# Optimization experiments

Hardware: AMD Instinct MI355X
Metric: run time of the kernel (lower is better)

The kernel has to match this reference:

```python
import jax, jax.numpy as jnp
import numpy as np

B, S, D, H, E = 4, 1024, 1024, 16, 4
HD = D // H
EPS = 1e-5


def setup_inputs() -> dict:
    key = jax.random.key(0)
    ks = jax.random.split(key, 6)
    std = 0.02
    return {
        "hidden_states": jax.random.normal(ks[0], (B, S, D), dtype=jnp.float32),
        "Wr": jax.random.normal(ks[1], (D, E), dtype=jnp.float32) * std,
        "br": jnp.zeros((E,), jnp.float32),
        "ln_g": jnp.ones((E, D), jnp.float32),
        "ln_b": jnp.zeros((E, D), jnp.float32),
        "W_attn": jax.random.normal(ks[2], (E, D, 3 * D), dtype=jnp.float32) * std,
        "b_attn": jnp.zeros((E, 3 * D), jnp.float32),
        "W_proj": jax.random.normal(ks[3], (E, D, D), dtype=jnp.float32) * std,
        "b_proj": jnp.zeros((E, D), jnp.float32),
    }


def reference(hidden_states, Wr, br, ln_g, ln_b, W_attn, b_attn, W_proj, b_proj):
    b, s, d = hidden_states.shape
    x = hidden_states.reshape(b * s, d)  # [N, D]

    # naive softmax router over experts
    score = jax.nn.softmax(x @ Wr + br, axis=-1)  # [N, E]

    # LayerNorm stats are expert-independent; affine is per-expert
    mu = jnp.mean(x, axis=-1, keepdims=True)
    var = jnp.mean(jnp.square(x - mu), axis=-1, keepdims=True)
    xn = (x - mu) * jax.lax.rsqrt(var + EPS)  # [N, D]

    ln_out = xn[:, None, :] * ln_g[None] + ln_b[None]  # [N, E, D]
    qkv_all = jnp.einsum('ned,edf->nef', ln_out, W_attn) + b_attn  # [N, E, 3D]
    # weighted_qkv: scale each expert's qkv by its routing score, sum
    qkv = jnp.einsum('ne,nef->nf', score, qkv_all)  # [N, 3D]

    q, k, v = jnp.split(qkv.reshape(b, s, 3 * d), 3, axis=-1)
    def split_heads(t):
        return t.reshape(b, s, H, HD).transpose(0, 2, 1, 3)  # [B,H,S,hd]
    q, k, v = split_heads(q), split_heads(k), split_heads(v)

    scale = 1.0 / jnp.sqrt(jnp.asarray(HD, q.dtype))
    att = jnp.einsum('bhqd,bhkd->bhqk', q, k) * scale  # [B,H,S,S]
    causal = jnp.tril(jnp.ones((s, s), dtype=bool))
    att = jnp.where(causal[None, None], att, jnp.finfo(att.dtype).min)
    probs = jax.nn.softmax(att, axis=-1)
    ctx = jnp.einsum('bhqk,bhkd->bhqd', probs, v)  # [B,H,S,hd]
    ctx = ctx.transpose(0, 2, 1, 3).reshape(b * s, d)  # [N, D]

    proj_all = jnp.einsum('nd,edf->nef', ctx, W_proj) + b_proj  # [N, E, D]
    out = jnp.einsum('ne,nef->nf', score, proj_all).reshape(b, s, d)
    return out
```

## Files before the change

kernel.cpp:

```cpp
#include <hip/hip_runtime.h>
#include <stdint.h>

#define NB 4
#define SS 1024
#define DD 1024
#define EE 4
#define HH 16
#define HDD 64
#define NN (NB*SS)
#define KK2 (EE*DD)
#define FF1 (3*DD)

typedef __attribute__((ext_vector_type(4))) float f32x4;
typedef __attribute__((ext_vector_type(8))) _Float16 half8;
typedef __attribute__((ext_vector_type(4))) _Float16 half4;

static __device__ __forceinline__ f32x4 mfma16(half8 a, half8 b, f32x4 c){
  return __builtin_amdgcn_mfma_f32_16x16x32_f16(a, b, c, 0, 0, 0);
}

#define GLOAD_LDS16(gp, lp) __builtin_amdgcn_global_load_lds( \
    (const unsigned int __attribute__((address_space(1)))*)(uintptr_t)(gp), \
    (unsigned int __attribute__((address_space(3)))*)(uintptr_t)(lp), 16, 0, 0)

#define SBAR() do { asm volatile("" ::: "memory"); \
                    __builtin_amdgcn_s_barrier(); \
                    asm volatile("" ::: "memory"); } while(0)
#define VMC(n) asm volatile("s_waitcnt vmcnt(" #n ")" ::: "memory")

__device__ __forceinline__ void prep_body(
    const float* __restrict__ x, const float* __restrict__ Wr,
    const float* __restrict__ br, float* __restrict__ score,
    float* __restrict__ ratios, _Float16* __restrict__ xnb,
    int n, float (*red)[6])
{
  int tid = threadIdx.x;
  float4 xv = ((const float4*)(x + (size_t)n*DD))[tid];
  float xa[4] = {xv.x, xv.y, xv.z, xv.w};
  float vals[6];
  vals[0] = xa[0]+xa[1]+xa[2]+xa[3];
  vals[1] = xa[0]*xa[0]+xa[1]*xa[1]+xa[2]*xa[2]+xa[3]*xa[3];
  vals[2] = vals[3] = vals[4] = vals[5] = 0.f;
  #pragma unroll
  for (int j = 0; j < 4; ++j){
    float4 w = ((const float4*)Wr)[tid*4 + j];
    vals[2] += xa[j]*w.x; vals[3] += xa[j]*w.y;
    vals[4] += xa[j]*w.z; vals[5] += xa[j]*w.w;
  }
  #pragma unroll
  for (int off = 32; off >= 1; off >>= 1)
    #pragma unroll
    for (int i = 0; i < 6; ++i)
      vals[i] += __shfl_xor(vals[i], off, 64);
  int wid = tid >> 6;
  if ((tid & 63) == 0){
    #pragma unroll
    for (int i = 0; i < 6; ++i) red[wid][i] = vals[i];
  }
  __syncthreads();
  float tot[6];
  #pragma unroll
  for (int i = 0; i < 6; ++i)
    tot[i] = red[0][i] + red[1][i] + red[2][i] + red[3][i];

  float mu   = tot[0] * (1.f/DD);
  float var  = tot[1] * (1.f/DD) - mu*mu;
  float rsig = rsqrtf(var + 1e-5f);
  float lg[4];
  #pragma unroll
  for (int e = 0; e < 4; ++e) lg[e] = tot[2+e] + br[e];
  float mx = fmaxf(fmaxf(lg[0], lg[1]), fmaxf(lg[2], lg[3]));
  float ex[4], esum = 0.f;
  #pragma unroll
  for (int e = 0; e < 4; ++e){ ex[e] = __expf(lg[e] - mx); esum += ex[e]; }
  if (tid < 4){
    score[n*4 + tid] = ex[tid] / esum;
    ratios[n*4 + tid] = (tid == 0) ? (ex[0] / esum) : (ex[tid] / ex[tid-1]);
  }

  half4 o;
  #pragma unroll
  for (int j = 0; j < 4; ++j) o[j] = (_Float16)((xa[j] - mu) * rsig);
  *(half4*)(xnb + (size_t)n*DD + tid*4) = o;
}

template<bool AFFINE>
__device__ __forceinline__ void transpose_body(
    const float* __restrict__ W, _Float16* __restrict__ WT, int K, int F,
    const float* __restrict__ gvec, const float* __restrict__ bvec,
    float* __restrict__ part, int k0, int f0,
    float (*t)[65], float (*red2)[64])
{
  int tid = threadIdx.x;
  int r = tid >> 4, c4 = (tid & 15) * 4;
  float pf[4] = {0.f, 0.f, 0.f, 0.f};
  #pragma unroll
  for (int i = 0; i < 4; ++i){
    int k = k0 + i*16 + r;
    float4 v = *(const float4*)(W + (size_t)k*F + f0 + c4);
    if constexpr (AFFINE){
      float bk = bvec[k];
      pf[0] += bk*v.x; pf[1] += bk*v.y; pf[2] += bk*v.z; pf[3] += bk*v.w;
      float gk = gvec[k];
      v.x *= gk; v.y *= gk; v.z *= gk; v.w *= gk;
    }
    t[i*16 + r][c4+0] = v.x; t[i*16 + r][c4+1] = v.y;
    t[i*16 + r][c4+2] = v.z; t[i*16 + r][c4+3] = v.w;
  }
  if constexpr (AFFINE){
    #pragma unroll
    for (int j = 0; j < 4; ++j) red2[r][c4+j] = pf[j];
  }
  __syncthreads();
  int f = tid >> 2, seg = tid & 3;
  half8 o0, o1;
  #pragma unroll
  for (int j = 0; j < 8; ++j){
    o0[j] = (_Float16)t[seg*16 + j][f];
    o1[j] = (_Float16)t[seg*16 + 8 + j][f];
  }
  _Float16* dst = WT + (size_t)(f0 + f)*K + k0 + seg*16;
  *(half8*)dst = o0;
  *(half8*)(dst + 8) = o1;
  if constexpr (AFFINE){
    if (tid < 64){
      float s = 0.f;
      #pragma unroll
      for (int rr = 0; rr < 16; ++rr) s += red2[rr][tid];
      part[(size_t)(k0/64) * F + f0 + tid] = s;
    }
  }
}

__global__ __launch_bounds__(256) void prep_fused_kernel(
    const float* __restrict__ W1, _Float16* __restrict__ W1T,
    const float* __restrict__ W2, _Float16* __restrict__ W2T,
    const float* __restrict__ gvec, const float* __restrict__ bvec,
    float* __restrict__ part,
    const float* __restrict__ x, const float* __restrict__ Wr,
    const float* __restrict__ br, float* __restrict__ score,
    float* __restrict__ ratios, _Float16* __restrict__ xnb)
{
  __shared__ float t[64][65];
  __shared__ float red2[16][64];
  __shared__ float red[4][6];
  int id = blockIdx.x;
  if (id & 1){
    prep_body(x, Wr, br, score, ratios, xnb, id >> 1, red);
  } else {
    int tr = id >> 1;
    int k0 = (tr & 63) * 64;
    int y  = tr >> 6;
    if (y < FF1/64)
      transpose_body<true >(W1, W1T, KK2, FF1, gvec, bvec, part, k0, y*64, t, red2);
    else
      transpose_body<false>(W2, W2T, KK2, DD, nullptr, nullptr, nullptr,
                            k0, (y - FF1/64)*64, t, red2);
  }
}

__global__ __launch_bounds__(256) void bb1_kernel(
    const float* __restrict__ b_attn, const float* __restrict__ part,
    float* __restrict__ BB1)
{
  int idx = blockIdx.x*256 + threadIdx.x;
  int e = idx / FF1, f = idx - e*FF1;
  float s = b_attn[idx];
  #pragma unroll
  for (int i = 0; i < 16; ++i)
    s += part[(size_t)(e*16 + i)*FF1 + f];
  BB1[idx] = s;
}

#define G1_BM 256
#define G1_BN 192
#define G1_BK 64
#define G1_NT 16
#define G1_ABUF (G1_BM*G1_BK)
#define G1_BBUF (G1_BN*G1_BK)

__global__ __launch_bounds__(512, 2) void gemm1_kernel(
    const _Float16* __restrict__ XN, const _Float16* __restrict__ BT,
    const float* __restrict__ score, const float* __restrict__ ratios,
    const float* __restrict__ bias, _Float16* __restrict__ C)
{
  __shared__ _Float16 smA[2*G1_ABUF];
  __shared__ _Float16 smB[3*G1_BBUF];
  int tid = threadIdx.x;
  int lane = tid & 63, wid = tid >> 6;
  int q = lane & 15, g = lane >> 4;
  int wr = wid >> 1, wc = wid & 1;
  int xo = (q & 7) << 3;
  int bid = blockIdx.x;
  int xcd = bid & 7, li = bid >> 3;
  int m0 = (li >> 1) * G1_BM;
  int n0 = (xcd*2 + (li & 1)) * G1_BN;

  int arow[4], brow[6];
  #pragma unroll
  for (int mf = 0; mf < 4; ++mf) arow[mf] = (wr*64 + mf*16 + q)*64;
  #pragma unroll
  for (int nf = 0; nf < 6; ++nf) brow[nf] = (wc*96 + nf*16 + q)*64;
  int soff[2] = { (g*8) ^ xo, (32 + g*8) ^ xo };

  _Float16 rf[4][4];
  #pragma unroll
  for (int mf = 0; mf < 4; ++mf){
    float4 rr = *(const float4*)(ratios + (size_t)(m0 + wr*64 + mf*16 + q)*4);
    rf[mf][0] = (_Float16)rr.x; rf[mf][1] = (_Float16)rr.y;
    rf[mf][2] = (_Float16)rr.z; rf[mf][3] = (_Float16)rr.w;
  }

  auto stageA = [&](int t){
    _Float16* sA = smA + (t & 1)*G1_ABUF;
    const int d0 = t * G1_BK;
    #pragma unroll
    for (int ld = 0; ld < 4; ++ld){
      int c = ld*512 + tid;
      int row = c >> 3;
      int seg = (c & 7) ^ (row & 7);
      GLOAD_LDS16(XN + (size_t)(m0 + row)*DD + d0 + seg*8,
                  sA + (ld*512 + wid*64)*8);
    }
  };
  auto stageB = [&](int gec){
    const int k0 = (gec & 3)*DD + (gec >> 2)*G1_BK;
    _Float16* sB = smB + (gec % 3)*G1_BBUF;
    #pragma unroll
    for (int ld = 0; ld < 3; ++ld){
      int c = ld*512 + tid;
      int row = c >> 3;
      int seg = (c & 7) ^ (row & 7);
      GLOAD_LDS16(BT + (size_t)(n0 + row)*KK2 + k0 + seg*8,
                  sB + (ld*512 + wid*64)*8);
    }
  };

  f32x4 acc[4][6] = {};
  half8 af[4][2];

  auto phase = [&](const _Float16* Ab, const _Float16* Bb,
                   _Float16 s0, _Float16 s1, _Float16 s2, _Float16 s3,
                   bool readAF){
    if (readAF){
      #pragma unroll
      for (int m = 0; m < 4; ++m)
        #pragma unroll
        for (int k = 0; k < 2; ++k)
          af[m][k] = *(const half8*)(Ab + arow[m] + soff[k]);
    }
    #pragma unroll
    for (int k = 0; k < 2; ++k)
      #pragma unroll
      for (int j = 0; j < 8; ++j){
        af[0][k][j] *= s0; af[1][k][j] *= s1;
        af[2][k][j] *= s2; af[3][k][j] *= s3;
      }
    half8 bf[3][2];
    #pragma unroll
    for (int n = 0; n < 3; ++n)
      #pragma unroll
      for (int k = 0; k < 2; ++k)
        bf[n][k] = *(const half8*)(Bb + brow[n] + soff[k]);
    __builtin_amdgcn_s_setprio(1);
    #pragma unroll
    for (int k = 0; k < 2; ++k)
      #pragma unroll
      for (int m = 0; m < 4; ++m)
        #pragma unroll
        for (int n = 0; n < 3; ++n)
          acc[m][n] = mfma16(af[m][k], bf[n][k], acc[m][n]);
    __builtin_amdgcn_s_setprio(0);
    #pragma unroll
    for (int n = 0; n < 3; ++n)
      #pragma unroll
      for (int k = 0; k < 2; ++k)
        bf[n][k] = *(const half8*)(Bb + brow[3+n] + soff[k]);
    __builtin_amdgcn_s_setprio(1);
    #pragma unroll
    for (int k = 0; k < 2; ++k)
      #pragma unroll
      for (int m = 0; m < 4; ++m)
        #pragma unroll
        for (int n = 0; n < 3; ++n)
          acc[m][3+n] = mfma16(af[m][k], bf[n][k], acc[m][3+n]);
    __builtin_amdgcn_s_setprio(0);
  };

  stageA(0); stageB(0); stageB(1);

  #pragma unroll 1
  for (int t = 0; t < G1_NT-1; ++t){
    const _Float16* Ab = smA + (t & 1)*G1_ABUF;
    int g4 = t*4;
    VMC(3); SBAR();
    stageB(g4+2);
    phase(Ab, smB + (g4 % 3)*G1_BBUF, rf[0][0], rf[1][0], rf[2][0], rf[3][0], true);
    VMC(3); SBAR();
    stageB(g4+3);
    phase(Ab, smB + ((g4+1) % 3)*G1_BBUF, rf[0][1], rf[1][1], rf[2][1], rf[3][1], false);
    VMC(3); SBAR();
    stageB(g4+4); stageA(t+1);
    phase(Ab, smB + ((g4+2) % 3)*G1_BBUF, rf[0][2], rf[1][2], rf[2][2], rf[3][2], false);
    VMC(7); SBAR();
    stageB(g4+5);
    phase(Ab, smB + ((g4+3) % 3)*G1_BBUF, rf[0][3], rf[1][3], rf[2][3], rf[3][3], false);
  }
  {
    const _Float16* Ab = smA + ((G1_NT-1) & 1)*G1_ABUF;
    VMC(3); SBAR();
    stageB(62);
    phase(Ab, smB + (60 % 3)*G1_BBUF, rf[0][0], rf[1][0], rf[2][0], rf[3][0], true);
    VMC(3); SBAR();
    stageB(63);
    phase(Ab, smB + (61 % 3)*G1_BBUF, rf[0][1], rf[1][1], rf[2][1], rf[3][1], false);
    VMC(3); SBAR();
    phase(Ab, smB + (62 % 3)*G1_BBUF, rf[0][2], rf[1][2], rf[2][2], rf[3][2], false);
    VMC(0); SBAR();
    phase(Ab, smB + (63 % 3)*G1_BBUF, rf[0][3], rf[1][3], rf[2][3], rf[3][3], false);
  }

  float bv[6][4];
  #pragma unroll
  for (int nf = 0; nf < 6; ++nf){
    int gn = n0 + wc*96 + nf*16 + q;
    #pragma unroll
    for (int e = 0; e < 4; ++e) bv[nf][e] = bias[e*FF1 + gn];
  }
  #pragma unroll
  for (int mf = 0; mf < 4; ++mf){
    #pragma unroll
    for (int r = 0; r < 4; ++r){
      int gm = m0 + wr*64 + mf*16 + g*4 + r;
      float4 sc = *(const float4*)(score + gm*4);
      #pragma unroll
      for (int nf = 0; nf < 6; ++nf){
        int gn = n0 + wc*96 + nf*16 + q;
        float v = acc[mf][nf][r]
                + sc.x*bv[nf][0] + sc.y*bv[nf][1] + sc.z*bv[nf][2] + sc.w*bv[nf][3];
        C[(size_t)gm*FF1 + gn] = (_Float16)v;
      }
    }
  }
}

#define G2_BK 64
#define G2_ABUF (128*G2_BK)
#define G2_BUFSZ (2*G2_ABUF)

__global__ __launch_bounds__(512) void gemm2_kernel(
    const _Float16* __restrict__ CTX, const _Float16* __restrict__ BT,
    const float* __restrict__ score, const float* __restrict__ bias,
    float* __restrict__ Cout)
{
  __shared__ _Float16 smem[2*G2_BUFSZ];
  int tid = threadIdx.x;
  int lane = tid & 63, wid = tid >> 6;
  int q = lane & 15, g = lane >> 4;
  int wr = wid >> 2, wc = wid & 3;
  int xo = (q & 7) << 3;
  int bid = blockIdx.x;
  int xcd = bid >> 5, idx = bid & 31;
  int m0 = (xcd*4 + (idx >> 3)) * 128;
  int n0 = (idx & 7) * 128;

  int arow[4], brow[2];
  #pragma unroll
  for (int mf = 0; mf < 4; ++mf) arow[mf] = (wr*64 + mf*16 + q)*64;
  #pragma unroll
  for (int nf = 0; nf < 2; ++nf) brow[nf] = G2_ABUF + (wc*32 + nf*16 + q)*64;
  int soff[2] = { (g*8) ^ xo, (32 + g*8) ^ xo };

  auto stage = [&](int t, int buf){
    const int d0 = (t & 15) * G2_BK;
    const int k0 = t * G2_BK;
    _Float16* sA = smem + buf*G2_BUFSZ;
    _Float16* sB = sA + G2_ABUF;
    #pragma unroll
    for (int ld = 0; ld < 2; ++ld){
      int c = ld*512 + tid;
      int row = c >> 3;
      int seg = (c & 7) ^ (row & 7);
      GLOAD_LDS16(CTX + (size_t)(m0 + row)*DD + d0 + seg*8,
                  sA + (ld*512 + wid*64)*8);
    }
    #pragma unroll
    for (int ld = 0; ld < 2; ++ld){
      int c = ld*512 + tid;
      int row = c >> 3;
      int seg = (c & 7) ^ (row & 7);
      GLOAD_LDS16(BT + (size_t)(n0 + row)*KK2 + k0 + seg*8,
                  sB + (ld*512 + wid*64)*8);
    }
  };

  f32x4 accp[4][2] = {}, acco[4][2] = {};

  auto merge = [&](int e){
    #pragma unroll
    for (int m = 0; m < 4; ++m)
      #pragma unroll
      for (int r = 0; r < 4; ++r){
        int gm = m0 + wr*64 + m*16 + g*4 + r;
        float s = score[(size_t)gm*4 + e];
        #pragma unroll
        for (int n = 0; n < 2; ++n){
          acco[m][n][r] += s*accp[m][n][r];
          accp[m][n][r] = 0.f;
        }
      }
  };

  half8 af[4][2], bfr[2][2];
  auto reads = [&](const _Float16* base, int k){
    #pragma unroll
    for (int m = 0; m < 4; ++m)
      af[m][k] = *(const half8*)(base + arow[m] + soff[k]);
    #pragma unroll
    for (int n = 0; n < 2; ++n)
      bfr[n][k] = *(const half8*)(base + brow[n] + soff[k]);
  };
  auto mfmas = [&](int k){
    __builtin_amdgcn_s_setprio(1);
    #pragma unroll
    for (int m = 0; m < 4; ++m)
      #pragma unroll
      for (int n = 0; n < 2; ++n)
        accp[m][n] = mfma16(af[m][k], bfr[n][k], accp[m][n]);
    __builtin_amdgcn_s_setprio(0);
  };

  stage(0, 0);
  for (int t = 0; t < KK2/G2_BK - 1; ++t){
    const _Float16* base = smem + (t & 1)*G2_BUFSZ;
    stage(t+1, (t+1)&1);
    asm volatile("s_waitcnt vmcnt(4)" ::: "memory");
    SBAR();
    reads(base, 0);
    mfmas(0);
    reads(base, 1);
    SBAR();
    mfmas(1);
    if ((t & 15) == 15) merge(t >> 4);
  }
  {
    const _Float16* base = smem + ((KK2/G2_BK - 1) & 1)*G2_BUFSZ;
    asm volatile("s_waitcnt vmcnt(0)" ::: "memory");
    SBAR();
    reads(base, 0); reads(base, 1);
    mfmas(0); mfmas(1);
    merge(3);
  }

  #pragma unroll
  for (int m = 0; m < 4; ++m){
    #pragma unroll
    for (int r = 0; r < 4; ++r){
      int gm = m0 + wr*64 + m*16 + g*4 + r;
      float4 sc = *(const float4*)(score + gm*4);
      #pragma unroll
      for (int n = 0; n < 2; ++n){
        int gn = n0 + wc*32 + n*16 + q;
        float v = acco[m][n][r]
                + sc.x*bias[gn] + sc.y*bias[DD+gn]
                + sc.z*bias[2*DD+gn] + sc.w*bias[3*DD+gn];
        Cout[(size_t)gm*DD + gn] = v;
      }
    }
  }
}

__global__ __launch_bounds__(512) void attn_kernel(
    const _Float16* __restrict__ qkv, _Float16* __restrict__ ctx)
{
  __shared__ _Float16 lsK[2][64*64];
  __shared__ _Float16 lsV[2][64*64];
  __shared__ _Float16 lsP[8][16*64];
  int id = blockIdx.x;
  int p = id >> 1, parity = id & 1;
  int bh = p & 63;
  int qtp = p >> 6;
  int qt = parity ? qtp : 7 - qtp;
  int b = bh >> 4, h = bh & 15;
  int tid = threadIdx.x, lane = tid & 63, wid = tid >> 6;
  int q = lane & 15, g = lane >> 4;
  int xo = (q & 7) << 3;
  int qrow0 = qt*128 + wid*16;

  half8 qf[2];
  #pragma unroll
  for (int kk = 0; kk < 2; ++kk)
    qf[kk] = *(const half8*)(qkv + ((size_t)b*SS + qrow0 + q)*FF1 + h*HDD + kk*32 + g*8);

  auto issueK = [&](int kt, int buf){
    size_t kvrow = (size_t)b*SS + kt*64;
    int row = tid >> 3, seg = (tid & 7) ^ (row & 7);
    GLOAD_LDS16(qkv + (kvrow + row)*FF1 + DD + h*HDD + seg*8,
                lsK[buf] + (size_t)(wid*64)*8);
  };
  auto issueV = [&](int kt, half8& vr){
    size_t kvrow = (size_t)b*SS + kt*64;
    vr = *(const half8*)(qkv + (kvrow + lane)*FF1 + 2*DD + h*HDD + wid*8);
  };
  auto writeV = [&](half8 vr, int buf){
    #pragma unroll
    for (int j = 0; j < 8; ++j){
      int hd = wid*8 + j;
      lsV[buf][hd*64 + (lane ^ ((hd & 7) << 3))] = vr[j];
    }
  };

  f32x4 o[4] = {};
  float mrow = -1e30f, lsum = 0.f;
  const float SC2 = 0.18033688011112042f;
  int qglob = qrow0 + q;
  int ktmax = 2*qt + 1;

  half8 vr;
  issueK(0, 0);
  issueV(0, vr);

  for (int kt = 0; kt <= ktmax; ++kt){
    int cur = kt & 1, nxt = cur ^ 1;
    int tn = (kt < ktmax) ? kt+1 : ktmax;
    bool active = (kt*64 <= qrow0 + 15);
    asm volatile("s_waitcnt vmcnt(1)" ::: "memory");
    SBAR();

    f32x4 st[4] = {};
    if (active){
      __builtin_amdgcn_s_setprio(1);
      #pragma unroll
      for (int i = 0; i < 4; ++i){
        #pragma unroll
        for (int kk = 0; kk < 2; ++kk){
          half8 kf = *(const half8*)(lsK[cur] + (i*16 + q)*64 + ((kk*32 + g*8) ^ xo));
          st[i] = mfma16(kf, qf[kk], st[i]);
        }
      }
      __builtin_amdgcn_s_setprio(0);
    }
    issueK(tn, nxt);
    asm volatile("s_waitcnt vmcnt(1)" ::: "memory");
    writeV(vr, cur);

    _Float16 pb[16];
    bool resc = false;
    float psum = 0.f;
    if (active){
      float pvv[16]; float tm = -1e30f;
      if (kt*64 + 63 > qrow0){
        #pragma unroll
        for (int i = 0; i < 4; ++i)
          #pragma unroll
          for (int r = 0; r < 4; ++r){
            int kglob = kt*64 + i*16 + g*4 + r;
            float sv = (kglob <= qglob) ? st[i][r]*SC2 : -1e30f;
            pvv[i*4+r] = sv; tm = fmaxf(tm, sv);
          }
      } else {
        #pragma unroll
        for (int i = 0; i < 4; ++i)
          #pragma unroll
          for (int r = 0; r < 4; ++r){
            float sv = st[i][r]*SC2;
            pvv[i*4+r] = sv; tm = fmaxf(tm, sv);
          }
      }
      tm = fmaxf(tm, __shfl_xor(tm, 16, 64));
      tm = fmaxf(tm, __shfl_xor(tm, 32, 64));
      resc = !__all(tm <= mrow);
      float mnew = resc ? fmaxf(mrow, tm) : mrow;
      #pragma unroll
      for (int i = 0; i < 16; ++i){
        float p2 = exp2f(pvv[i] - mnew);
        psum += p2; pb[i] = (_Float16)p2;
      }
      if (resc){
        float alpha = exp2f(mrow - mnew);
        mrow = mnew;
        lsum = lsum*alpha + psum;
        float af4[4];
        #pragma unroll
        for (int r = 0; r < 4; ++r) af4[r] = __shfl(alpha, g*4 + r, 64);
        #pragma unroll
        for (int n = 0; n < 4; ++n)
          #pragma unroll
          for (int r = 0; r < 4; ++r) o[n][r] *= af4[r];
      } else {
        lsum += psum;
      }
    }
    issueV(tn, vr);

    asm volatile("s_waitcnt lgkmcnt(0)" ::: "memory");
    SBAR();

    if (active){
      #pragma unroll
      for (int i = 0; i < 4; ++i){
        half4 w4;
        w4[0]=pb[i*4+0]; w4[1]=pb[i*4+1]; w4[2]=pb[i*4+2]; w4[3]=pb[i*4+3];
        *(half4*)(&lsP[wid][q*64 + ((i*16 + g*4) ^ xo)]) = w4;
      }
      __builtin_amdgcn_s_setprio(1);
      #pragma unroll
      for (int kk = 0; kk < 2; ++kk){
        half8 pf = *(const half8*)(&lsP[wid][q*64 + ((kk*32 + g*8) ^ xo)]);
        #pragma unroll
        for (int n = 0; n < 4; ++n){
          half8 vf = *(const half8*)(&lsV[cur][(n*16 + q)*64 + ((kk*32 + g*8) ^ xo)]);
          o[n] = mfma16(pf, vf, o[n]);
        }
      }
      __builtin_amdgcn_s_setprio(0);
    }
  }
  float lt = lsum + __shfl_xor(lsum, 16, 64);
  lt = lt + __shfl_xor(lt, 32, 64);
  float rinv = 1.f / lt;
  #pragma unroll
  for (int r = 0; r < 4; ++r){
    float ri = __shfl(rinv, g*4 + r, 64);
    int qg = qt*128 + wid*16 + g*4 + r;
    _Float16* obase = ctx + ((size_t)b*SS + qg)*DD + h*HDD;
    #pragma unroll
    for (int n = 0; n < 4; ++n)
      obase[n*16 + q] = (_Float16)(o[n][r] * ri);
  }
}

extern "C" void kernel_launch(void* const* d_in, const int* in_sizes, int n_in,
                              void* d_out, int out_size, void* d_ws, size_t ws_size,
                              hipStream_t stream)
{
  const float* x      = (const float*)d_in[0];
  const float* Wr     = (const float*)d_in[1];
  const float* br     = (const float*)d_in[2];
  const float* ln_g   = (const float*)d_in[3];
  const float* ln_b   = (const float*)d_in[4];
  const float* W_attn = (const float*)d_in[5];
  const float* b_attn = (const float*)d_in[6];
  const float* W_proj = (const float*)d_in[7];
  const float* b_proj = (const float*)d_in[8];
  (void)in_sizes; (void)n_in; (void)out_size; (void)ws_size;

  char* ws = (char*)d_ws;
  size_t off = 0;
  auto alloc = [&](size_t bytes) -> void* {
    void* p = ws + off; off += (bytes + 255) & ~(size_t)255; return p;
  };
  _Float16* W1gT  = (_Float16*)alloc((size_t)FF1*KK2*2);
  _Float16* W2T   = (_Float16*)alloc((size_t)DD*KK2*2);
  float*    score = (float*)   alloc((size_t)NN*4*4);
  float*    ratio = (float*)   alloc((size_t)NN*4*4);
  _Float16* xn16  = (_Float16*)alloc((size_t)NN*DD*2);
  _Float16* qkv   = (_Float16*)alloc((size_t)NN*FF1*2);
  _Float16* ctx   = (_Float16*)alloc((size_t)NN*DD*2);
  float*    part  = (float*)   alloc((size_t)(KK2/64)*FF1*4);
  float*    BB1   = (float*)   alloc((size_t)EE*FF1*4);

  hipLaunchKernelGGL(prep_fused_kernel, dim3(8192), dim3(256), 0, stream,
                     W_attn, W1gT, W_proj, W2T, ln_g, ln_b, part,
                     x, Wr, br, score, ratio, xn16);
  hipLaunchKernelGGL(bb1_kernel, dim3(EE*FF1/256), dim3(256), 0, stream,
                     b_attn, part, BB1);
  hipLaunchKernelGGL(gemm1_kernel, dim3(256), dim3(512), 0, stream,
                     xn16, W1gT, score, ratio, BB1, qkv);
  hipLaunchKernelGGL(attn_kernel, dim3(512), dim3(512), 0, stream,
                     qkv, ctx);
  hipLaunchKernelGGL(gemm2_kernel, dim3(256), dim3(512), 0, stream,
                     ctx, W2T, score, b_proj, (float*)d_out);
}
```

Baseline: 197.4 us.

## Reuse CTX tile across experts in gemm2 with ratio-scaled A fragments

gemm2 now loads each CTX K-tile once into LDS and reuses it for all four experts. Before each expert's MFMAs it scales the A fragments in registers by a per-row fp16 ratio, so all experts accumulate into one accumulator and the per-expert score merge goes away. The B tiles use a three-deep LDS ring and launch bounds now request 4 waves per EU. This cuts CTX traffic and merge ALU work, but adds per-element fp16 multiplies on A and relies on fp16 ratios, which brings rounding risk.

```diff
diff --git a/kernel.cpp b/kernel.cpp
--- a/kernel.cpp
+++ b/kernel.cpp
@@ -345,15 +345,17 @@
 }
 
 #define G2_BK 64
+#define G2_NT 16
 #define G2_ABUF (128*G2_BK)
-#define G2_BUFSZ (2*G2_ABUF)
-
-__global__ __launch_bounds__(512) void gemm2_kernel(
+#define G2_BBUF (128*G2_BK)
+
+__global__ __launch_bounds__(512, 4) void gemm2_kernel(
     const _Float16* __restrict__ CTX, const _Float16* __restrict__ BT,
-    const float* __restrict__ score, const float* __restrict__ bias,
-    float* __restrict__ Cout)
-{
-  __shared__ _Float16 smem[2*G2_BUFSZ];
+    const float* __restrict__ score, const float* __restrict__ ratios,
+    const float* __restrict__ bias, float* __restrict__ Cout)
+{
+  __shared__ _Float16 smA[2*G2_ABUF];
+  __shared__ _Float16 smB[3*G2_BBUF];
   int tid = threadIdx.x;
   int lane = tid & 63, wid = tid >> 6;
   int q = lane & 15, g = lane >> 4;
@@ -368,14 +370,20 @@
   #pragma unroll
   for (int mf = 0; mf < 4; ++mf) arow[mf] = (wr*64 + mf*16 + q)*64;
   #pragma unroll
-  for (int nf = 0; nf < 2; ++nf) brow[nf] = G2_ABUF + (wc*32 + nf*16 + q)*64;
+  for (int nf = 0; nf < 2; ++nf) brow[nf] = (wc*32 + nf*16 + q)*64;
   int soff[2] = { (g*8) ^ xo, (32 + g*8) ^ xo };
 
-  auto stage = [&](int t, int buf){
-    const int d0 = (t & 15) * G2_BK;
-    const int k0 = t * G2_BK;
-    _Float16* sA = smem + buf*G2_BUFSZ;
-    _Float16* sB = sA + G2_ABUF;
+  _Float16 rf[4][4];
+  #pragma unroll
+  for (int mf = 0; mf < 4; ++mf){
+    float4 rr = *(const float4*)(ratios + (size_t)(m0 + wr*64 + mf*16 + q)*4);
+    rf[mf][0] = (_Float16)rr.x; rf[mf][1] = (_Float16)rr.y;
+    rf[mf][2] = (_Float16)rr.z; rf[mf][3] = (_Float16)rr.w;
+  }
+
+  auto stageA = [&](int t){
+    _Float16* sA = smA + (t & 1)*G2_ABUF;
+    const int d0 = t * G2_BK;
     #pragma unroll
     for (int ld = 0; ld < 2; ++ld){
       int c = ld*512 + tid;
@@ -384,6 +392,10 @@
       GLOAD_LDS16(CTX + (size_t)(m0 + row)*DD + d0 + seg*8,
                   sA + (ld*512 + wid*64)*8);
     }
+  };
+  auto stageB = [&](int gec){
+    const int k0 = (gec & 3)*DD + (gec >> 2)*G2_BK;
+    _Float16* sB = smB + (gec % 3)*G2_BBUF;
     #pragma unroll
     for (int ld = 0; ld < 2; ++ld){
       int c = ld*512 + tid;
@@ -394,62 +406,74 @@
     }
   };
 
-  f32x4 accp[4][2] = {}, acco[4][2] = {};
-
-  auto merge = [&](int e){
-    #pragma unroll
-    for (int m = 0; m < 4; ++m)
-      #pragma unroll
-      for (int r = 0; r < 4; ++r){
-        int gm = m0 + wr*64 + m*16 + g*4 + r;
-        float s = score[(size_t)gm*4 + e];
-        #pragma unroll
-        for (int n = 0; n < 2; ++n){
-          acco[m][n][r] += s*accp[m][n][r];
-          accp[m][n][r] = 0.f;
-        }
-      }
-  };
-
-  half8 af[4][2], bfr[2][2];
-  auto reads = [&](const _Float16* base, int k){
-    #pragma unroll
-    for (int m = 0; m < 4; ++m)
-      af[m][k] = *(const half8*)(base + arow[m] + soff[k]);
+  f32x4 acc[4][2] = {};
+  half8 af[4][2];
+
+  auto phase = [&](const _Float16* Ab, const _Float16* Bb,
+                   _Float16 s0, _Float16 s1, _Float16 s2, _Float16 s3,
+                   bool readAF){
+    if (readAF){
+      #pragma unroll
+      for (int m = 0; m < 4; ++m)
+        #pragma unroll
+        for (int k = 0; k < 2; ++k)
+          af[m][k] = *(const half8*)(Ab + arow[m] + soff[k]);
+    }
+    #pragma unroll
+    for (int k = 0; k < 2; ++k)
+      #pragma unroll
+      for (int j = 0; j < 8; ++j){
+        af[0][k][j] *= s0; af[1][k][j] *= s1;
+        af[2][k][j] *= s2; af[3][k][j] *= s3;
+      }
+    half8 bf[2][2];
     #pragma unroll
     for (int n = 0; n < 2; ++n)
-      bfr[n][k] = *(const half8*)(base + brow[n] + soff[k]);
-  };
-  auto mfmas = [&](int k){
+      #pragma unroll
+      for (int k = 0; k < 2; ++k)
+        bf[n][k] = *(const half8*)(Bb + brow[n] + soff[k]);
     __builtin_amdgcn_s_setprio(1);
     #pragma unroll
-    for (int m = 0; m < 4; ++m)
-      #pragma unroll
-      for (int n = 0; n < 2; ++n)
-        accp[m][n] = mfma16(af[m][k], bfr[n][k], accp[m][n]);
+    for (int k = 0; k < 2; ++k)
+      #pragma unroll
+      for (int m = 0; m < 4; ++m)
+        #pragma unroll
+        for (int n = 0; n < 2; ++n)
+          acc[m][n] = mfma16(af[m][k], bf[n][k], acc[m][n]);
     __builtin_amdgcn_s_setprio(0);
   };
 
-  stage(0, 0);
-  for (int t = 0; t < KK2/G2_BK - 1; ++t){
-    const _Float16* base = smem + (t & 1)*G2_BUFSZ;
-    stage(t+1, (t+1)&1);
-    asm volatile("s_waitcnt vmcnt(4)" ::: "memory");
-    SBAR();
-    reads(base, 0);
-    mfmas(0);
-    reads(base, 1);
-    SBAR();
-    mfmas(1);
-    if ((t & 15) == 15) merge(t >> 4);
+  stageA(0); stageB(0); stageB(1);
+
+  #pragma unroll 1
+  for (int t = 0; t < G2_NT-1; ++t){
+    const _Float16* Ab = smA + (t & 1)*G2_ABUF;
+    int g4 = t*4;
+    VMC(2); SBAR();
+    stageB(g4+2);
+    phase(Ab, smB + (g4 % 3)*G2_BBUF, rf[0][0], rf[1][0], rf[2][0], rf[3][0], true);
+    VMC(2); SBAR();
+    stageB(g4+3);
+    phase(Ab, smB + ((g4+1) % 3)*G2_BBUF, rf[0][1], rf[1][1], rf[2][1], rf[3][1], false);
+    VMC(2); SBAR();
+    stageB(g4+4); stageA(t+1);
+    phase(Ab, smB + ((g4+2) % 3)*G2_BBUF, rf[0][2], rf[1][2], rf[2][2], rf[3][2], false);
+    VMC(4); SBAR();
+    stageB(g4+5);
+    phase(Ab, smB + ((g4+3) % 3)*G2_BBUF, rf[0][3], rf[1][3], rf[2][3], rf[3][3], false);
   }
   {
-    const _Float16* base = smem + ((KK2/G2_BK - 1) & 1)*G2_BUFSZ;
-    asm volatile("s_waitcnt vmcnt(0)" ::: "memory");
-    SBAR();
-    reads(base, 0); reads(base, 1);
-    mfmas(0); mfmas(1);
-    merge(3);
+    const _Float16* Ab = smA + ((G2_NT-1) & 1)*G2_ABUF;
+    VMC(2); SBAR();
+    stageB(62);
+    phase(Ab, smB + (60 % 3)*G2_BBUF, rf[0][0], rf[1][0], rf[2][0], rf[3][0], true);
+    VMC(2); SBAR();
+    stageB(63);
+    phase(Ab, smB + (61 % 3)*G2_BBUF, rf[0][1], rf[1][1], rf[2][1], rf[3][1], false);
+    VMC(2); SBAR();
+    phase(Ab, smB + (62 % 3)*G2_BBUF, rf[0][2], rf[1][2], rf[2][2], rf[3][2], false);
+    VMC(0); SBAR();
+    phase(Ab, smB + (63 % 3)*G2_BBUF, rf[0][3], rf[1][3], rf[2][3], rf[3][3], false);
   }
 
   #pragma unroll
@@ -461,7 +485,7 @@
       #pragma unroll
       for (int n = 0; n < 2; ++n){
         int gn = n0 + wc*32 + n*16 + q;
-        float v = acco[m][n][r]
+        float v = acc[m][n][r]
                 + sc.x*bias[gn] + sc.y*bias[DD+gn]
                 + sc.z*bias[2*DD+gn] + sc.w*bias[3*DD+gn];
         Cout[(size_t)gm*DD + gn] = v;
@@ -670,5 +694,5 @@
   hipLaunchKernelGGL(attn_kernel, dim3(512), dim3(512), 0, stream,
                      qkv, ctx);
   hipLaunchKernelGGL(gemm2_kernel, dim3(256), dim3(512), 0, stream,
-                     ctx, W2T, score, b_proj, (float*)d_out);
-}
+                     ctx, W2T, score, ratio, b_proj, (float*)d_out);
+}
```

Measured after the change: 201.8 us. 1.02x slower.
